# Kernel tuning notes

Hardware: AMD Instinct MI355X
Metric: run time of the kernel (lower is better)

The kernel has to match this reference:

```python
import jax, jax.numpy as jnp
import numpy as np

NUM_USERS = 100000
NUM_ITEMS = 100000
SEQ_LEN = 32
EMBED_DIM = 64
FC_DIM = 100
BATCH = 512
T = 3  # number of target items per example (train mode)


def setup_inputs() -> dict:
    key = jax.random.key(0)
    ks = jax.random.split(key, 12)
    seq_var = jax.random.randint(ks[0], (BATCH, SEQ_LEN), 0, NUM_ITEMS)
    user_var = jax.random.randint(ks[1], (BATCH, 1), 0, NUM_USERS)
    item_var = jax.random.randint(ks[2], (BATCH, T), 0, NUM_ITEMS)
    # Embedding tables, init normal(0, 1/dim) as in the torch module
    item_emb = jax.random.normal(ks[3], (NUM_ITEMS, EMBED_DIM)) * (1.0 / EMBED_DIM)
    user_emb = jax.random.normal(ks[4], (NUM_USERS, EMBED_DIM)) * (1.0 / EMBED_DIM)
    W2 = jax.random.normal(ks[5], (NUM_ITEMS, FC_DIM + EMBED_DIM)) * (1.0 / (FC_DIM + EMBED_DIM))
    b2 = jnp.zeros((NUM_ITEMS, 1))
    # nn.Linear default init: U(-1/sqrt(fan_in), 1/sqrt(fan_in))
    lim1 = 1.0 / np.sqrt(2 * EMBED_DIM)
    W1 = jax.random.uniform(ks[6], (FC_DIM, 2 * EMBED_DIM), minval=-lim1, maxval=lim1)
    b1 = jax.random.uniform(ks[7], (FC_DIM,), minval=-lim1, maxval=lim1)
    lim2 = 1.0 / np.sqrt(FC_DIM)
    Wf2 = jax.random.uniform(ks[8], (FC_DIM, FC_DIM), minval=-lim2, maxval=lim2)
    bf2 = jax.random.uniform(ks[9], (FC_DIM,), minval=-lim2, maxval=lim2)
    return dict(seq_var=seq_var, user_var=user_var, item_var=item_var,
                item_emb=item_emb, user_emb=user_emb, W2=W2, b2=b2,
                W1=W1, b1=b1, Wf2=Wf2, bf2=bf2)


def reference(seq_var, user_var, item_var, item_emb, user_emb, W2, b2, W1, b1, Wf2, bf2):
    # Dropout is identity in eval mode.
    d = item_emb.shape[1]
    embs = item_emb[seq_var]          # [B, L, d]
    uemb = user_emb[user_var]         # [B, 1, d]
    # fc1 on concat(item_i, item_j): split W1 columns so we never build the
    # [B, L, L, 2d] concat tensor; same math as Linear(cat([i, j])).
    Wa, Wb = W1[:, :d], W1[:, d:]     # [FC, d] each
    # all_embed[b, a, c] = cat(embs[b, c], embs[b, a])  (item_i varies with c)
    A = jnp.einsum('bld,fd->blf', embs, Wa)   # applied to item_i (index c)
    Bm = jnp.einsum('bld,fd->blf', embs, Wb)  # applied to item_j (index a)
    h = jax.nn.relu(A[:, None, :, :] + Bm[:, :, None, :] + b1)  # [B, L, L, FC]
    h = jax.nn.relu(jnp.einsum('bacf,gf->bacg', h, Wf2) + bf2)  # [B, L, L, FC]
    x = h.sum((1, 2))                               # [B, FC]
    x = jnp.concatenate([x, uemb[:, 0, :]], axis=1)  # [B, FC + d]
    w2 = W2[item_var]                                # [B, T, FC+d]
    bb = b2[item_var]                                # [B, T, 1]
    out = bb[..., 0] + jnp.einsum('btf,bf->bt', w2, x)  # baddbmm + squeeze -> [B, T]
    return out
```

## Files before the change

### kernel.cpp

```cpp
#include <hip/hip_runtime.h>
#include <hip/hip_bf16.h>

typedef float f32x4 __attribute__((ext_vector_type(4)));
typedef short short8 __attribute__((ext_vector_type(8)));

#define SEQ_LEN 32
#define EMBED_DIM 64
#define FC_DIM 100
#define BATCH 512
#define AS 132
#define ES 80

union FragAB { short8 s; __bf16 h[8]; };

__global__ __launch_bounds__(256, 2) void cosrec_fused(
    const int* __restrict__ seq_var, const int* __restrict__ user_var,
    const int* __restrict__ item_var, const float* __restrict__ item_emb,
    const float* __restrict__ user_emb, const float* __restrict__ W2,
    const float* __restrict__ b2, const float* __restrict__ W1,
    const float* __restrict__ b1, const float* __restrict__ Wf2,
    const float* __restrict__ bf2, float* __restrict__ out)
{
  __shared__ __align__(16) float A_s[SEQ_LEN * AS];
  __shared__ __align__(16) float B_s[SEQ_LEN * AS];
  __shared__ float red_s[16 * 112];
  __shared__ float x_s[112];
  __shared__ __align__(16) __bf16 emb_s[SEQ_LEN * ES];

  const int b = blockIdx.x;
  const int t = threadIdx.x;
  const int w = t >> 6;
  const int l = t & 63;
  const int l15 = l & 15;
  const int q = l >> 4;

  FragAB wfrag[7][4];
  #pragma unroll
  for (int nt = 0; nt < 7; ++nt) {
    const int gg = nt * 16 + l15;
    #pragma unroll
    for (int ks = 0; ks < 4; ++ks) {
      const int f0 = ks * 32 + q * 8;
      if (gg < FC_DIM && ks < 3) {
        const float4 u0 = *(const float4*)(Wf2 + gg * FC_DIM + f0);
        const float4 u1 = *(const float4*)(Wf2 + gg * FC_DIM + f0 + 4);
        wfrag[nt][ks].h[0] = (__bf16)u0.x; wfrag[nt][ks].h[1] = (__bf16)u0.y;
        wfrag[nt][ks].h[2] = (__bf16)u0.z; wfrag[nt][ks].h[3] = (__bf16)u0.w;
        wfrag[nt][ks].h[4] = (__bf16)u1.x; wfrag[nt][ks].h[5] = (__bf16)u1.y;
        wfrag[nt][ks].h[6] = (__bf16)u1.z; wfrag[nt][ks].h[7] = (__bf16)u1.w;
      } else {
        #pragma unroll
        for (int j = 0; j < 8; ++j) {
          const int f = f0 + j;
          wfrag[nt][ks].h[j] = (gg < FC_DIM && f < FC_DIM)
                                   ? (__bf16)Wf2[gg * FC_DIM + f] : (__bf16)0.0f;
        }
      }
    }
  }
  float bf2r[7];
  #pragma unroll
  for (int nt = 0; nt < 7; ++nt) {
    const int gg = nt * 16 + l15;
    bf2r[nt] = (gg < FC_DIM) ? bf2[gg] : 0.0f;
  }

  {
    const int r = t >> 3;
    const int c0 = (t & 7) * 8;
    const int item = seq_var[b * SEQ_LEN + r];
    const float4 v0 = *(const float4*)(item_emb + item * EMBED_DIM + c0);
    const float4 v1 = *(const float4*)(item_emb + item * EMBED_DIM + c0 + 4);
    FragAB e;
    e.h[0] = (__bf16)v0.x; e.h[1] = (__bf16)v0.y;
    e.h[2] = (__bf16)v0.z; e.h[3] = (__bf16)v0.w;
    e.h[4] = (__bf16)v1.x; e.h[5] = (__bf16)v1.y;
    e.h[6] = (__bf16)v1.z; e.h[7] = (__bf16)v1.w;
    *(short8*)(emb_s + r * ES + c0) = e.s;
  }
  for (int i = t; i < SEQ_LEN * 32; i += 256) {
    const int r = i >> 5, c = FC_DIM + (i & 31);
    A_s[r * AS + c] = 0.f;
    B_s[r * AS + c] = 0.f;
  }
  __syncthreads();

  for (int nt = w; nt < 13; nt += 4) {
    const int o = nt * 16 + l15;
    int wr = 0, wc = 0;
    bool valid = true;
    if (o < FC_DIM)            { wr = o;          wc = 0;  }
    else if (o < 2 * FC_DIM)   { wr = o - FC_DIM; wc = 64; }
    else valid = false;
    FragAB bfr[2];
    #pragma unroll
    for (int ks = 0; ks < 2; ++ks) {
      if (valid) {
        const float* p = W1 + wr * 128 + wc + ks * 32 + q * 8;
        const float4 u0 = *(const float4*)p;
        const float4 u1 = *(const float4*)(p + 4);
        bfr[ks].h[0] = (__bf16)u0.x; bfr[ks].h[1] = (__bf16)u0.y;
        bfr[ks].h[2] = (__bf16)u0.z; bfr[ks].h[3] = (__bf16)u0.w;
        bfr[ks].h[4] = (__bf16)u1.x; bfr[ks].h[5] = (__bf16)u1.y;
        bfr[ks].h[6] = (__bf16)u1.z; bfr[ks].h[7] = (__bf16)u1.w;
      } else {
        #pragma unroll
        for (int j = 0; j < 8; ++j) bfr[ks].h[j] = (__bf16)0.0f;
      }
    }
    const float b1v = (o >= FC_DIM && o < 2 * FC_DIM) ? b1[o - FC_DIM] : 0.f;
    #pragma unroll
    for (int mt = 0; mt < 2; ++mt) {
      FragAB afr[2];
      #pragma unroll
      for (int ks = 0; ks < 2; ++ks)
        afr[ks].s = *(const short8*)(emb_s + (mt * 16 + l15) * ES + ks * 32 + q * 8);
      f32x4 acc = {0.f, 0.f, 0.f, 0.f};
      #pragma unroll
      for (int ks = 0; ks < 2; ++ks)
        acc = __builtin_amdgcn_mfma_f32_16x16x32_bf16(afr[ks].s, bfr[ks].s, acc, 0, 0, 0);
      const int row = mt * 16 + q * 4;
      if (o < FC_DIM) {
        #pragma unroll
        for (int r = 0; r < 4; ++r) A_s[(row + r) * AS + o] = acc[r];
      } else if (o < 2 * FC_DIM) {
        #pragma unroll
        for (int r = 0; r < 4; ++r) B_s[(row + r) * AS + (o - FC_DIM)] = acc[r] + b1v;
      }
    }
  }
  __syncthreads();

  float colsum[7];
  #pragma unroll
  for (int nt = 0; nt < 7; ++nt) colsum[nt] = 0.f;

  for (int g = w; g < 8; g += 4) {
    const int c = (g & 1) * 16 + l15;
    const int a0 = (g >> 1) * 8;
    const float4* ap = (const float4*)(A_s + c * AS);
    float areg[32];
    #pragma unroll
    for (int ks = 0; ks < 4; ++ks) {
      const float4 v0 = ap[ks * 8 + q * 2];
      const float4 v1 = ap[ks * 8 + q * 2 + 1];
      areg[ks*8+0] = v0.x; areg[ks*8+1] = v0.y; areg[ks*8+2] = v0.z; areg[ks*8+3] = v0.w;
      areg[ks*8+4] = v1.x; areg[ks*8+5] = v1.y; areg[ks*8+6] = v1.z; areg[ks*8+7] = v1.w;
    }
    for (int ai = 0; ai < 8; ++ai) {
      const float4* bp = (const float4*)(B_s + (a0 + ai) * AS);
      FragAB hf[4];
      #pragma unroll
      for (int ks = 0; ks < 4; ++ks) {
        const float4 b0 = bp[ks * 8 + q * 2];
        const float4 b1f = bp[ks * 8 + q * 2 + 1];
        hf[ks].h[0] = (__bf16)fmaxf(areg[ks*8+0] + b0.x, 0.f);
        hf[ks].h[1] = (__bf16)fmaxf(areg[ks*8+1] + b0.y, 0.f);
        hf[ks].h[2] = (__bf16)fmaxf(areg[ks*8+2] + b0.z, 0.f);
        hf[ks].h[3] = (__bf16)fmaxf(areg[ks*8+3] + b0.w, 0.f);
        hf[ks].h[4] = (__bf16)fmaxf(areg[ks*8+4] + b1f.x, 0.f);
        hf[ks].h[5] = (__bf16)fmaxf(areg[ks*8+5] + b1f.y, 0.f);
        hf[ks].h[6] = (__bf16)fmaxf(areg[ks*8+6] + b1f.z, 0.f);
        hf[ks].h[7] = (__bf16)fmaxf(areg[ks*8+7] + b1f.w, 0.f);
      }
      #pragma unroll
      for (int nt = 0; nt < 7; ++nt) {
        f32x4 acc = {0.f, 0.f, 0.f, 0.f};
        #pragma unroll
        for (int ks = 0; ks < 4; ++ks)
          acc = __builtin_amdgcn_mfma_f32_16x16x32_bf16(hf[ks].s, wfrag[nt][ks].s, acc, 0, 0, 0);
        #pragma unroll
        for (int r = 0; r < 4; ++r)
          colsum[nt] += fmaxf(acc[r] + bf2r[nt], 0.f);
      }
    }
  }

  #pragma unroll
  for (int nt = 0; nt < 7; ++nt)
    red_s[(w * 4 + q) * 112 + nt * 16 + l15] = colsum[nt];
  __syncthreads();
  if (t < 112) {
    float s = 0.f;
    #pragma unroll
    for (int r = 0; r < 16; ++r) s += red_s[r * 112 + t];
    x_s[t] = s;
  }
  __syncthreads();

  float partial = 0.f;
  if (w < 3) {
    const int iv = item_var[b * 3 + w];
    const int uu = user_var[b];
    for (int idx = l; idx < FC_DIM + EMBED_DIM; idx += 64) {
      const float xv = (idx < FC_DIM)
                           ? x_s[idx]
                           : user_emb[uu * EMBED_DIM + (idx - FC_DIM)];
      partial += W2[iv * (FC_DIM + EMBED_DIM) + idx] * xv;
    }
  }
  red_s[w * 64 + l] = partial;
  __syncthreads();
  if (t < 3) {
    float s = 0.f;
    for (int i = 0; i < 64; ++i) s += red_s[t * 64 + i];
    const int iv = item_var[b * 3 + t];
    out[b * 3 + t] = s + b2[iv];
  }
}

extern "C" void kernel_launch(void* const* d_in, const int* in_sizes, int n_in,
                              void* d_out, int out_size, void* d_ws, size_t ws_size,
                              hipStream_t stream) {
  const int* seq = (const int*)d_in[0];
  const int* usr = (const int*)d_in[1];
  const int* itm = (const int*)d_in[2];
  const float* item_emb = (const float*)d_in[3];
  const float* user_emb = (const float*)d_in[4];
  const float* W2  = (const float*)d_in[5];
  const float* b2  = (const float*)d_in[6];
  const float* W1  = (const float*)d_in[7];
  const float* b1  = (const float*)d_in[8];
  const float* Wf2 = (const float*)d_in[9];
  const float* bf2 = (const float*)d_in[10];
  cosrec_fused<<<BATCH, 256, 0, stream>>>(seq, usr, itm, item_emb, user_emb,
                                          W2, b2, W1, b1, Wf2, bf2,
                                          (float*)d_out);
}
```

Before: 159.5 us.

## Switch to fp16 packed math, fold bias into MFMA, shuffle final reduction

Stores the fc1 outputs A/B in shared memory as fp16 instead of fp32 and computes the add+relu with packed half8 vector ops, removing the per-element fp32-to-bf16 conversions in the hot loop. Adds bf2 into the MFMA by setting a constant 1.0 in the padding column of the activation fragment and placing bf2 in the matching weight slot, which removes the per-element bias add. Replaces the shared-memory final dot-product reduction with wave shuffles. fp16 has less range than bf16, which is a possible precision concern.

```diff
diff --git a/kernel.cpp b/kernel.cpp
--- a/kernel.cpp
+++ b/kernel.cpp
@@ -1,17 +1,22 @@
 #include <hip/hip_runtime.h>
-#include <hip/hip_bf16.h>
 
 typedef float f32x4 __attribute__((ext_vector_type(4)));
 typedef short short8 __attribute__((ext_vector_type(8)));
+typedef _Float16 half8 __attribute__((ext_vector_type(8)));
 
 #define SEQ_LEN 32
 #define EMBED_DIM 64
 #define FC_DIM 100
 #define BATCH 512
-#define AS 132
-#define ES 80
-
-union FragAB { short8 s; __bf16 h[8]; };
+#define AS 136
+#define ES 72
+
+union Frag {
+  half8 h8;
+  _Float16 h[8];
+  short8 s;
+  unsigned int u[4];
+};
 
 __global__ __launch_bounds__(256, 2) void cosrec_fused(
     const int* __restrict__ seq_var, const int* __restrict__ user_var,
@@ -21,11 +26,11 @@
     const float* __restrict__ b1, const float* __restrict__ Wf2,
     const float* __restrict__ bf2, float* __restrict__ out)
 {
-  __shared__ __align__(16) float A_s[SEQ_LEN * AS];
-  __shared__ __align__(16) float B_s[SEQ_LEN * AS];
+  __shared__ __align__(16) _Float16 A_s[SEQ_LEN * AS];
+  __shared__ __align__(16) _Float16 B_s[SEQ_LEN * AS];
   __shared__ float red_s[16 * 112];
   __shared__ float x_s[112];
-  __shared__ __align__(16) __bf16 emb_s[SEQ_LEN * ES];
+  __shared__ __align__(16) _Float16 emb_s[SEQ_LEN * ES];
 
   const int b = blockIdx.x;
   const int t = threadIdx.x;
@@ -33,37 +38,7 @@
   const int l = t & 63;
   const int l15 = l & 15;
   const int q = l >> 4;
-
-  FragAB wfrag[7][4];
-  #pragma unroll
-  for (int nt = 0; nt < 7; ++nt) {
-    const int gg = nt * 16 + l15;
-    #pragma unroll
-    for (int ks = 0; ks < 4; ++ks) {
-      const int f0 = ks * 32 + q * 8;
-      if (gg < FC_DIM && ks < 3) {
-        const float4 u0 = *(const float4*)(Wf2 + gg * FC_DIM + f0);
-        const float4 u1 = *(const float4*)(Wf2 + gg * FC_DIM + f0 + 4);
-        wfrag[nt][ks].h[0] = (__bf16)u0.x; wfrag[nt][ks].h[1] = (__bf16)u0.y;
-        wfrag[nt][ks].h[2] = (__bf16)u0.z; wfrag[nt][ks].h[3] = (__bf16)u0.w;
-        wfrag[nt][ks].h[4] = (__bf16)u1.x; wfrag[nt][ks].h[5] = (__bf16)u1.y;
-        wfrag[nt][ks].h[6] = (__bf16)u1.z; wfrag[nt][ks].h[7] = (__bf16)u1.w;
-      } else {
-        #pragma unroll
-        for (int j = 0; j < 8; ++j) {
-          const int f = f0 + j;
-          wfrag[nt][ks].h[j] = (gg < FC_DIM && f < FC_DIM)
-                                   ? (__bf16)Wf2[gg * FC_DIM + f] : (__bf16)0.0f;
-        }
-      }
-    }
-  }
-  float bf2r[7];
-  #pragma unroll
-  for (int nt = 0; nt < 7; ++nt) {
-    const int gg = nt * 16 + l15;
-    bf2r[nt] = (gg < FC_DIM) ? bf2[gg] : 0.0f;
-  }
+  const unsigned int biasbits = (q == 0) ? 0x00003C00u : 0u;
 
   {
     const int r = t >> 3;
@@ -71,17 +46,48 @@
     const int item = seq_var[b * SEQ_LEN + r];
     const float4 v0 = *(const float4*)(item_emb + item * EMBED_DIM + c0);
     const float4 v1 = *(const float4*)(item_emb + item * EMBED_DIM + c0 + 4);
-    FragAB e;
-    e.h[0] = (__bf16)v0.x; e.h[1] = (__bf16)v0.y;
-    e.h[2] = (__bf16)v0.z; e.h[3] = (__bf16)v0.w;
-    e.h[4] = (__bf16)v1.x; e.h[5] = (__bf16)v1.y;
-    e.h[6] = (__bf16)v1.z; e.h[7] = (__bf16)v1.w;
+    Frag e;
+    e.h[0] = (_Float16)v0.x; e.h[1] = (_Float16)v0.y;
+    e.h[2] = (_Float16)v0.z; e.h[3] = (_Float16)v0.w;
+    e.h[4] = (_Float16)v1.x; e.h[5] = (_Float16)v1.y;
+    e.h[6] = (_Float16)v1.z; e.h[7] = (_Float16)v1.w;
     *(short8*)(emb_s + r * ES + c0) = e.s;
   }
-  for (int i = t; i < SEQ_LEN * 32; i += 256) {
-    const int r = i >> 5, c = FC_DIM + (i & 31);
-    A_s[r * AS + c] = 0.f;
-    B_s[r * AS + c] = 0.f;
+  for (int i = t; i < SEQ_LEN * 14; i += 256) {
+    const int r = i / 14, d = (i % 14) * 2;
+    *(unsigned int*)(A_s + r * AS + FC_DIM + d) = 0u;
+    *(unsigned int*)(B_s + r * AS + FC_DIM + d) = 0u;
+  }
+
+  Frag wfrag[7][4];
+  #pragma unroll
+  for (int nt = 0; nt < 7; ++nt) {
+    const int gg = nt * 16 + l15;
+    const bool gok = (gg < FC_DIM);
+    #pragma unroll
+    for (int ks = 0; ks < 3; ++ks) {
+      Frag f;
+      if (gok) {
+        const float4 u0 = *(const float4*)(Wf2 + gg * FC_DIM + ks * 32 + q * 8);
+        const float4 u1 = *(const float4*)(Wf2 + gg * FC_DIM + ks * 32 + q * 8 + 4);
+        f.h[0] = (_Float16)u0.x; f.h[1] = (_Float16)u0.y;
+        f.h[2] = (_Float16)u0.z; f.h[3] = (_Float16)u0.w;
+        f.h[4] = (_Float16)u1.x; f.h[5] = (_Float16)u1.y;
+        f.h[6] = (_Float16)u1.z; f.h[7] = (_Float16)u1.w;
+      } else {
+        f.u[0] = 0u; f.u[1] = 0u; f.u[2] = 0u; f.u[3] = 0u;
+      }
+      wfrag[nt][ks] = f;
+    }
+    Frag f3;
+    f3.u[0] = 0u; f3.u[1] = 0u; f3.u[2] = 0u; f3.u[3] = 0u;
+    if (gok && q == 0) {
+      const float4 u0 = *(const float4*)(Wf2 + gg * FC_DIM + 96);
+      f3.h[0] = (_Float16)u0.x; f3.h[1] = (_Float16)u0.y;
+      f3.h[2] = (_Float16)u0.z; f3.h[3] = (_Float16)u0.w;
+      f3.h[4] = (_Float16)bf2[gg];
+    }
+    wfrag[nt][3] = f3;
   }
   __syncthreads();
 
@@ -92,40 +98,41 @@
     if (o < FC_DIM)            { wr = o;          wc = 0;  }
     else if (o < 2 * FC_DIM)   { wr = o - FC_DIM; wc = 64; }
     else valid = false;
-    FragAB bfr[2];
+    Frag bfr[2];
     #pragma unroll
     for (int ks = 0; ks < 2; ++ks) {
       if (valid) {
         const float* p = W1 + wr * 128 + wc + ks * 32 + q * 8;
         const float4 u0 = *(const float4*)p;
         const float4 u1 = *(const float4*)(p + 4);
-        bfr[ks].h[0] = (__bf16)u0.x; bfr[ks].h[1] = (__bf16)u0.y;
-        bfr[ks].h[2] = (__bf16)u0.z; bfr[ks].h[3] = (__bf16)u0.w;
-        bfr[ks].h[4] = (__bf16)u1.x; bfr[ks].h[5] = (__bf16)u1.y;
-        bfr[ks].h[6] = (__bf16)u1.z; bfr[ks].h[7] = (__bf16)u1.w;
+        bfr[ks].h[0] = (_Float16)u0.x; bfr[ks].h[1] = (_Float16)u0.y;
+        bfr[ks].h[2] = (_Float16)u0.z; bfr[ks].h[3] = (_Float16)u0.w;
+        bfr[ks].h[4] = (_Float16)u1.x; bfr[ks].h[5] = (_Float16)u1.y;
+        bfr[ks].h[6] = (_Float16)u1.z; bfr[ks].h[7] = (_Float16)u1.w;
       } else {
-        #pragma unroll
-        for (int j = 0; j < 8; ++j) bfr[ks].h[j] = (__bf16)0.0f;
+        bfr[ks].u[0] = 0u; bfr[ks].u[1] = 0u; bfr[ks].u[2] = 0u; bfr[ks].u[3] = 0u;
       }
     }
     const float b1v = (o >= FC_DIM && o < 2 * FC_DIM) ? b1[o - FC_DIM] : 0.f;
     #pragma unroll
     for (int mt = 0; mt < 2; ++mt) {
-      FragAB afr[2];
+      Frag afr[2];
       #pragma unroll
       for (int ks = 0; ks < 2; ++ks)
         afr[ks].s = *(const short8*)(emb_s + (mt * 16 + l15) * ES + ks * 32 + q * 8);
       f32x4 acc = {0.f, 0.f, 0.f, 0.f};
       #pragma unroll
       for (int ks = 0; ks < 2; ++ks)
-        acc = __builtin_amdgcn_mfma_f32_16x16x32_bf16(afr[ks].s, bfr[ks].s, acc, 0, 0, 0);
+        acc = __builtin_amdgcn_mfma_f32_16x16x32_f16(afr[ks].h8, bfr[ks].h8, acc, 0, 0, 0);
       const int row = mt * 16 + q * 4;
       if (o < FC_DIM) {
         #pragma unroll
-        for (int r = 0; r < 4; ++r) A_s[(row + r) * AS + o] = acc[r];
+        for (int r = 0; r < 4; ++r)
+          A_s[(row + r) * AS + o] = (_Float16)acc[r];
       } else if (o < 2 * FC_DIM) {
         #pragma unroll
-        for (int r = 0; r < 4; ++r) B_s[(row + r) * AS + (o - FC_DIM)] = acc[r] + b1v;
+        for (int r = 0; r < 4; ++r)
+          B_s[(row + r) * AS + (o - FC_DIM)] = (_Float16)(acc[r] + b1v);
       }
     }
   }
@@ -134,44 +141,35 @@
   float colsum[7];
   #pragma unroll
   for (int nt = 0; nt < 7; ++nt) colsum[nt] = 0.f;
+  const half8 hzero = {};
 
   for (int g = w; g < 8; g += 4) {
     const int c = (g & 1) * 16 + l15;
     const int a0 = (g >> 1) * 8;
-    const float4* ap = (const float4*)(A_s + c * AS);
-    float areg[32];
-    #pragma unroll
-    for (int ks = 0; ks < 4; ++ks) {
-      const float4 v0 = ap[ks * 8 + q * 2];
-      const float4 v1 = ap[ks * 8 + q * 2 + 1];
-      areg[ks*8+0] = v0.x; areg[ks*8+1] = v0.y; areg[ks*8+2] = v0.z; areg[ks*8+3] = v0.w;
-      areg[ks*8+4] = v1.x; areg[ks*8+5] = v1.y; areg[ks*8+6] = v1.z; areg[ks*8+7] = v1.w;
-    }
+    Frag areg[4];
+    #pragma unroll
+    for (int ks = 0; ks < 4; ++ks)
+      areg[ks].s = *(const short8*)(A_s + c * AS + ks * 32 + q * 8);
     for (int ai = 0; ai < 8; ++ai) {
-      const float4* bp = (const float4*)(B_s + (a0 + ai) * AS);
-      FragAB hf[4];
+      const _Float16* bp = B_s + (a0 + ai) * AS;
+      Frag hf[4];
       #pragma unroll
       for (int ks = 0; ks < 4; ++ks) {
-        const float4 b0 = bp[ks * 8 + q * 2];
-        const float4 b1f = bp[ks * 8 + q * 2 + 1];
-        hf[ks].h[0] = (__bf16)fmaxf(areg[ks*8+0] + b0.x, 0.f);
-        hf[ks].h[1] = (__bf16)fmaxf(areg[ks*8+1] + b0.y, 0.f);
-        hf[ks].h[2] = (__bf16)fmaxf(areg[ks*8+2] + b0.z, 0.f);
-        hf[ks].h[3] = (__bf16)fmaxf(areg[ks*8+3] + b0.w, 0.f);
-        hf[ks].h[4] = (__bf16)fmaxf(areg[ks*8+4] + b1f.x, 0.f);
-        hf[ks].h[5] = (__bf16)fmaxf(areg[ks*8+5] + b1f.y, 0.f);
-        hf[ks].h[6] = (__bf16)fmaxf(areg[ks*8+6] + b1f.z, 0.f);
-        hf[ks].h[7] = (__bf16)fmaxf(areg[ks*8+7] + b1f.w, 0.f);
-      }
+        Frag br;
+        br.s = *(const short8*)(bp + ks * 32 + q * 8);
+        const half8 sum = areg[ks].h8 + br.h8;
+        hf[ks].h8 = __builtin_elementwise_max(sum, hzero);
+      }
+      hf[3].u[2] |= biasbits;
       #pragma unroll
       for (int nt = 0; nt < 7; ++nt) {
         f32x4 acc = {0.f, 0.f, 0.f, 0.f};
         #pragma unroll
         for (int ks = 0; ks < 4; ++ks)
-          acc = __builtin_amdgcn_mfma_f32_16x16x32_bf16(hf[ks].s, wfrag[nt][ks].s, acc, 0, 0, 0);
+          acc = __builtin_amdgcn_mfma_f32_16x16x32_f16(hf[ks].h8, wfrag[nt][ks].h8, acc, 0, 0, 0);
         #pragma unroll
         for (int r = 0; r < 4; ++r)
-          colsum[nt] += fmaxf(acc[r] + bf2r[nt], 0.f);
+          colsum[nt] += fmaxf(acc[r], 0.f);
       }
     }
   }
@@ -188,24 +186,20 @@
   }
   __syncthreads();
 
-  float partial = 0.f;
   if (w < 3) {
     const int iv = item_var[b * 3 + w];
     const int uu = user_var[b];
+    float partial = 0.f;
     for (int idx = l; idx < FC_DIM + EMBED_DIM; idx += 64) {
       const float xv = (idx < FC_DIM)
                            ? x_s[idx]
                            : user_emb[uu * EMBED_DIM + (idx - FC_DIM)];
       partial += W2[iv * (FC_DIM + EMBED_DIM) + idx] * xv;
     }
-  }
-  red_s[w * 64 + l] = partial;
-  __syncthreads();
-  if (t < 3) {
-    float s = 0.f;
-    for (int i = 0; i < 64; ++i) s += red_s[t * 64 + i];
-    const int iv = item_var[b * 3 + t];
-    out[b * 3 + t] = s + b2[iv];
+    #pragma unroll
+    for (int off = 32; off > 0; off >>= 1)
+      partial += __shfl_down(partial, off, 64);
+    if (l == 0) out[b * 3 + w] = partial + b2[iv];
   }
 }
 
```

Measured after the change: 157.1 us. About the same (-1.5%).
